# Kernel optimization log

Hardware: AMD Instinct MI355X
Metric: run time of the kernel (lower is better)

Reference implementation:

```python
import jax, jax.numpy as jnp
import numpy as np

IN_DIM, OUT_DIM, HID, L, PRED_LEN = 6, 6, 512, 4, 10


def _rnn_layer(x, Wih, Whh, bih, bhh):
    """Vanilla tanh RNN layer, batch_first x: [B,T,D] -> ([B,T,H], hT [B,H])."""
    B = x.shape[0]
    H = Whh.shape[0]
    xW = jnp.einsum('btd,hd->bth', x, Wih) + bih  # precompute input projections

    def step(h, xw_t):
        h = jnp.tanh(xw_t + h @ Whh.T + bhh)
        return h, h

    h0 = jnp.zeros((B, H), x.dtype)
    hT, ys = jax.lax.scan(step, h0, jnp.swapaxes(xW, 0, 1))
    return jnp.swapaxes(ys, 0, 1), hT


def setup_inputs() -> dict:
    key = jax.random.key(0)
    ks = jax.random.split(key, 16)
    s_in = 1.0 / np.sqrt(HID)
    u = lambda k, shp: jax.random.uniform(k, shp, jnp.float32, -s_in, s_in)
    inp = {
        'x': jax.random.normal(ks[0], (1024, 128, IN_DIM), jnp.float32),
        # encoder RNN params (layer 0 has input_dim=6, layers 1..3 have HID)
        'enc_Wih0': u(ks[1], (HID, IN_DIM)),
        'enc_Wih': u(ks[2], (L - 1, HID, HID)),
        'enc_Whh': u(ks[3], (L, HID, HID)),
        'enc_bih': u(ks[4], (L, HID)),
        'enc_bhh': u(ks[5], (L, HID)),
        # decoder RNN params (all layers take HID-dim input)
        'dec_Wih': u(ks[6], (L, HID, HID)),
        'dec_Whh': u(ks[7], (L, HID, HID)),
        'dec_bih': u(ks[8], (L, HID)),
        'dec_bhh': u(ks[9], (L, HID)),
        # output head
        'fc_W': u(ks[10], (OUT_DIM, HID)),
        'fc_b': u(ks[11], (OUT_DIM,)),
    }
    return inp


def reference(x, enc_Wih0, enc_Wih, enc_Whh, enc_bih, enc_bhh,
              dec_Wih, dec_Whh, dec_bih, dec_bhh, fc_W, fc_b):
    B = x.shape[0]
    # ---- encoder: 4-layer tanh RNN over src sequence ----
    h_enc = []
    out = x
    for l in range(L):
        Wih = enc_Wih0 if l == 0 else enc_Wih[l - 1]
        out, hT = _rnn_layer(out, Wih, enc_Whh[l], enc_bih[l], enc_bhh[l])
        h_enc.append(hT)
    enc_outputs = out                      # [B, T_src, HID]
    hidden = jnp.stack(h_enc)              # [L, B, HID]

    de_input0 = enc_outputs[:, -1, :]      # [B, HID]

    def dec_step(carry, _):
        inp, h = carry
        x_l = inp
        new_h = []
        for l in range(L):
            hl = jnp.tanh(x_l @ dec_Wih[l].T + dec_bih[l]
                          + h[l] @ dec_Whh[l].T + dec_bhh[l])
            new_h.append(hl)
            x_l = hl
        return (x_l, jnp.stack(new_h)), x_l

    _, ys = jax.lax.scan(dec_step, (de_input0, hidden), None, length=PRED_LEN)
    dec_out = jnp.swapaxes(ys, 0, 1)       # [B, PRED_LEN, HID]
    outputs = dec_out @ fc_W.T + fc_b      # [B, PRED_LEN, OUT_DIM]
    return enc_outputs, outputs
```

## Files before the change

kernel.cpp:

```cpp
#include <hip/hip_runtime.h>

typedef _Float16 f16;
typedef _Float16 f16x8 __attribute__((ext_vector_type(8)));
typedef float    f32x4 __attribute__((ext_vector_type(4)));
typedef unsigned long long u64;

#define TSEQ 128
#define PRED 10

__global__ void k_cvt(const float* __restrict__ src, f16* __restrict__ dst, int n) {
  int i = blockIdx.x * blockDim.x + threadIdx.x;
  int stride = gridDim.x * blockDim.x;
  for (; i < n; i += stride) dst[i] = (f16)src[i];
}

__global__ void k_bias(const float* __restrict__ a, const float* __restrict__ b,
                       float* __restrict__ o, int n) {
  int i = blockIdx.x * blockDim.x + threadIdx.x;
  if (i < n) o[i] = a[i] + b[i];
}

__global__ __launch_bounds__(256) void k_gemm_xw(
    const f16* __restrict__ A, const f16* __restrict__ W,
    const float* __restrict__ bias, f16* __restrict__ C) {
  __shared__ f16 As[128 * 72];
  __shared__ f16 Bs[256 * 72];
  const int tid = threadIdx.x;
  const int w = tid >> 6, lane = tid & 63;
  const int wm = w >> 1, wn = w & 1;
  const int q = lane >> 4, l15 = lane & 15;
  const int m0 = blockIdx.x * 128;
  const int n0 = blockIdx.y * 256;

  f32x4 acc[4][8];
  const f32x4 zero = {0.f, 0.f, 0.f, 0.f};
#pragma unroll
  for (int i = 0; i < 4; i++)
#pragma unroll
    for (int j = 0; j < 8; j++) acc[i][j] = zero;

  for (int k0 = 0; k0 < 512; k0 += 64) {
    __syncthreads();
#pragma unroll
    for (int i = 0; i < 4; i++) {
      int ch = tid + 256 * i; int r = ch >> 3, kc = ch & 7;
      *(f16x8*)&As[r * 72 + kc * 8] = *(const f16x8*)&A[(size_t)(m0 + r) * 512 + k0 + kc * 8];
    }
#pragma unroll
    for (int i = 0; i < 8; i++) {
      int ch = tid + 256 * i; int r = ch >> 3, kc = ch & 7;
      *(f16x8*)&Bs[r * 72 + kc * 8] = *(const f16x8*)&W[(size_t)(n0 + r) * 512 + k0 + kc * 8];
    }
    __syncthreads();
#pragma unroll
    for (int kk = 0; kk < 2; kk++) {
      f16x8 af[4], bf[8];
#pragma unroll
      for (int mt = 0; mt < 4; mt++)
        af[mt] = *(const f16x8*)&As[(wm * 64 + mt * 16 + l15) * 72 + kk * 32 + q * 8];
#pragma unroll
      for (int nt = 0; nt < 8; nt++)
        bf[nt] = *(const f16x8*)&Bs[(wn * 128 + nt * 16 + l15) * 72 + kk * 32 + q * 8];
#pragma unroll
      for (int mt = 0; mt < 4; mt++)
#pragma unroll
        for (int nt = 0; nt < 8; nt++)
          acc[mt][nt] = __builtin_amdgcn_mfma_f32_16x16x32_f16(af[mt], bf[nt], acc[mt][nt], 0, 0, 0);
    }
  }
#pragma unroll
  for (int mt = 0; mt < 4; mt++)
#pragma unroll
    for (int nt = 0; nt < 8; nt++)
#pragma unroll
      for (int r = 0; r < 4; r++) {
        int mg = m0 + wm * 64 + mt * 16 + q * 4 + r;
        int ng = n0 + wn * 128 + nt * 16 + l15;
        C[(size_t)mg * 512 + ng] = (f16)(acc[mt][nt][r] + bias[ng]);
      }
}

__global__ __launch_bounds__(256) void k_enc_rec(
    const f16* __restrict__ xw, const float* __restrict__ x,
    const float* __restrict__ Wih0, const float* __restrict__ bias0,
    const f16* __restrict__ Whh, f16* __restrict__ out_h,
    float* __restrict__ out_f, f16* __restrict__ hT,
    f16* __restrict__ hx, int* __restrict__ ctr, int is_l0) {
  __shared__ f16 As[16 * 520];
  __shared__ float xs[16][8];
  const int tid = threadIdx.x;
  const int w = tid >> 6, lane = tid & 63, q = lane >> 4, l15 = lane & 15;
  const int c = blockIdx.x & 63, sub = blockIdx.x >> 6;
  const int row0 = c * 16;
  const int ncol0 = sub * 128 + w * 32;
  int* myctr = ctr + c * 32;

  f16x8 Bfr[2][16];
#pragma unroll
  for (int t2 = 0; t2 < 2; t2++) {
    int ng = ncol0 + t2 * 16 + l15;
#pragma unroll
    for (int kk = 0; kk < 16; kk++)
      Bfr[t2][kk] = *(const f16x8*)&Whh[(size_t)ng * 512 + kk * 32 + q * 8];
  }

  float w0[2][6]; float b0[2];
  if (is_l0) {
#pragma unroll
    for (int t2 = 0; t2 < 2; t2++) {
      int ng = ncol0 + t2 * 16 + l15;
#pragma unroll
      for (int d = 0; d < 6; d++) w0[t2][d] = Wih0[ng * 6 + d];
      b0[t2] = bias0[ng];
    }
  }

  for (int i = tid; i < 16 * 520; i += 256) As[i] = (f16)0.0f;
  if (is_l0 && tid < 96) xs[tid / 6][tid % 6] = x[(size_t)(row0 + tid / 6) * TSEQ * 6 + tid % 6];
  __syncthreads();

  for (int t = 0; t < TSEQ; t++) {
    const int p = t & 1;
    f16 xwr[2][4];
    if (!is_l0) {
#pragma unroll
      for (int t2 = 0; t2 < 2; t2++)
#pragma unroll
        for (int r = 0; r < 4; r++)
          xwr[t2][r] = xw[((size_t)(row0 + q * 4 + r) * TSEQ + t) * 512 + ncol0 + t2 * 16 + l15];
    }

    const f32x4 zero = {0.f, 0.f, 0.f, 0.f};
    f32x4 acc0 = zero, acc1 = zero;
#pragma unroll
    for (int kk = 0; kk < 16; kk++) {
      f16x8 a = *(const f16x8*)&As[l15 * 520 + kk * 32 + q * 8];
      acc0 = __builtin_amdgcn_mfma_f32_16x16x32_f16(a, Bfr[0][kk], acc0, 0, 0, 0);
      acc1 = __builtin_amdgcn_mfma_f32_16x16x32_f16(a, Bfr[1][kk], acc1, 0, 0, 0);
    }

    float hv[2][4];
    union { u64 u; f16 h4[4]; } pk[2];
#pragma unroll
    for (int t2 = 0; t2 < 2; t2++) {
      f32x4 accv = t2 ? acc1 : acc0;
#pragma unroll
      for (int r = 0; r < 4; r++) {
        int m = q * 4 + r;
        float pre;
        if (is_l0) {
          float xwv = b0[t2];
#pragma unroll
          for (int d = 0; d < 6; d++) xwv += xs[m][d] * w0[t2][d];
          pre = accv[r] + xwv;
        } else {
          pre = accv[r] + (float)xwr[t2][r];
        }
        hv[t2][r] = tanhf(pre);
        pk[t2].h4[r] = (f16)hv[t2][r];
      }
    }

    if (t < TSEQ - 1) {
#pragma unroll
      for (int t2 = 0; t2 < 2; t2++) {
        int ng = ncol0 + t2 * 16 + l15;
        __hip_atomic_store(
            (u64*)&hx[(((size_t)p * 64 + c) * 512 + ng) * 16 + q * 4],
            pk[t2].u, __ATOMIC_RELAXED, __HIP_MEMORY_SCOPE_AGENT);
      }
      __builtin_amdgcn_s_waitcnt(0);
      __syncthreads();
      if (tid == 0)
        __hip_atomic_fetch_add(myctr, 1, __ATOMIC_RELAXED, __HIP_MEMORY_SCOPE_AGENT);
    }

#pragma unroll
    for (int t2 = 0; t2 < 2; t2++) {
      int ng = ncol0 + t2 * 16 + l15;
#pragma unroll
      for (int r = 0; r < 4; r++) {
        int b = row0 + q * 4 + r;
        out_h[((size_t)b * TSEQ + t) * 512 + ng] = pk[t2].h4[r];
        if (out_f) out_f[((size_t)b * TSEQ + t) * 512 + ng] = hv[t2][r];
        if (t == TSEQ - 1) hT[(size_t)b * 512 + ng] = pk[t2].h4[r];
      }
    }
    if (t == TSEQ - 1) break;

    if (tid == 0) {
      int target = 4 * (t + 1);
      while (__hip_atomic_load(myctr, __ATOMIC_RELAXED, __HIP_MEMORY_SCOPE_AGENT) < target)
        __builtin_amdgcn_s_sleep(1);
    }
    __syncthreads();

    {
      u64 v[8];
#pragma unroll
      for (int cc = 0; cc < 2; cc++) {
        int col = tid * 2 + cc;
        const u64* bp = (const u64*)&hx[(((size_t)p * 64 + c) * 512 + col) * 16];
#pragma unroll
        for (int j = 0; j < 4; j++)
          v[cc * 4 + j] = __hip_atomic_load(bp + j, __ATOMIC_RELAXED, __HIP_MEMORY_SCOPE_AGENT);
      }
      union { u64 u[4]; f16 h[16]; } un0, un1;
      un0.u[0] = v[0]; un0.u[1] = v[1]; un0.u[2] = v[2]; un0.u[3] = v[3];
      un1.u[0] = v[4]; un1.u[1] = v[5]; un1.u[2] = v[6]; un1.u[3] = v[7];
#pragma unroll
      for (int k = 0; k < 16; k++) {
        union { f16 h2[2]; unsigned int u; } pw;
        pw.h2[0] = un0.h[k]; pw.h2[1] = un1.h[k];
        *(unsigned int*)&As[k * 520 + tid * 2] = pw.u;
      }
    }
    if (is_l0 && tid < 96)
      xs[tid / 6][tid % 6] = x[((size_t)(row0 + tid / 6) * TSEQ + (t + 1)) * 6 + tid % 6];
    __syncthreads();
  }
}

__global__ __launch_bounds__(256) void k_dec_rec(
    const f16* __restrict__ Wih, const f16* __restrict__ Whh,
    const float* __restrict__ decB, const f16* __restrict__ hT,
    f16* __restrict__ hstate, f16* __restrict__ dec_out, int* __restrict__ ctr) {
  __shared__ f16 xb[16 * 520];
  __shared__ f16 hb[16 * 520];
  const int tid = threadIdx.x;
  const int w = tid >> 6, lane = tid & 63, q = lane >> 4, l15 = lane & 15;
  const int c = blockIdx.x >> 2, sub = blockIdx.x & 3;
  const int row0 = c * 16;
  const int ncol0 = sub * 128 + w * 32;
  int* myctr = ctr + c * 32;
  const size_t LSZ = (size_t)1024 * 512;

  auto load_rm = [&](f16* dst, const f16* src) {
#pragma unroll
    for (int i = 0; i < 4; i++) {
      int idx = tid + 256 * i; int m = idx >> 6, kc = idx & 63;
      *(f16x8*)&dst[m * 520 + kc * 8] = *(const f16x8*)&src[(size_t)(row0 + m) * 512 + kc * 8];
    }
  };
  auto load_cm = [&](f16* dst, int buf) {
    u64 v[8];
#pragma unroll
    for (int cc = 0; cc < 2; cc++) {
      int col = tid * 2 + cc;
      const u64* bp = (const u64*)&hstate[(((size_t)buf * 64 + c) * 512 + col) * 16];
#pragma unroll
      for (int j = 0; j < 4; j++)
        v[cc * 4 + j] = __hip_atomic_load(bp + j, __ATOMIC_RELAXED, __HIP_MEMORY_SCOPE_AGENT);
    }
    union { u64 u[4]; f16 h[16]; } un0, un1;
    un0.u[0] = v[0]; un0.u[1] = v[1]; un0.u[2] = v[2]; un0.u[3] = v[3];
    un1.u[0] = v[4]; un1.u[1] = v[5]; un1.u[2] = v[6]; un1.u[3] = v[7];
#pragma unroll
    for (int k = 0; k < 16; k++) {
      union { f16 h2[2]; unsigned int u; } pw;
      pw.h2[0] = un0.h[k]; pw.h2[1] = un1.h[k];
      *(unsigned int*)&dst[k * 520 + tid * 2] = pw.u;
    }
  };

  for (int s = 0; s < PRED; s++) {
    int wb = (s + 1) & 1, rb = s & 1;
    for (int l = 0; l < 4; l++) {
      const bool last = (s == PRED - 1) && (l == 3);
      if (l == 0) {
        if (s == 0) load_rm(xb, hT + 3 * LSZ);
        else load_cm(xb, rb * 4 + 3);
      } else {
        load_cm(xb, wb * 4 + (l - 1));
      }
      if (s == 0) load_rm(hb, hT + (size_t)l * LSZ);
      else load_cm(hb, rb * 4 + l);
      __syncthreads();

      const f32x4 zero = {0.f, 0.f, 0.f, 0.f};
      f32x4 acc0 = zero, acc1 = zero;
      const f16* Wl = Wih + (size_t)l * 512 * 512;
      const f16* Ul = Whh + (size_t)l * 512 * 512;
      int ng0 = ncol0 + l15, ng1 = ncol0 + 16 + l15;
#pragma unroll
      for (int kk = 0; kk < 16; kk++) {
        f16x8 a = *(const f16x8*)&xb[l15 * 520 + kk * 32 + q * 8];
        f16x8 bv0 = *(const f16x8*)&Wl[(size_t)ng0 * 512 + kk * 32 + q * 8];
        f16x8 bv1 = *(const f16x8*)&Wl[(size_t)ng1 * 512 + kk * 32 + q * 8];
        acc0 = __builtin_amdgcn_mfma_f32_16x16x32_f16(a, bv0, acc0, 0, 0, 0);
        acc1 = __builtin_amdgcn_mfma_f32_16x16x32_f16(a, bv1, acc1, 0, 0, 0);
      }
#pragma unroll
      for (int kk = 0; kk < 16; kk++) {
        f16x8 a = *(const f16x8*)&hb[l15 * 520 + kk * 32 + q * 8];
        f16x8 bv0 = *(const f16x8*)&Ul[(size_t)ng0 * 512 + kk * 32 + q * 8];
        f16x8 bv1 = *(const f16x8*)&Ul[(size_t)ng1 * 512 + kk * 32 + q * 8];
        acc0 = __builtin_amdgcn_mfma_f32_16x16x32_f16(a, bv0, acc0, 0, 0, 0);
        acc1 = __builtin_amdgcn_mfma_f32_16x16x32_f16(a, bv1, acc1, 0, 0, 0);
      }

      int obuf = wb * 4 + l;
      union { u64 u; f16 h4[4]; } pk[2];
#pragma unroll
      for (int t2 = 0; t2 < 2; t2++) {
        f32x4 accv = t2 ? acc1 : acc0;
        int ng = ncol0 + t2 * 16 + l15;
#pragma unroll
        for (int r = 0; r < 4; r++)
          pk[t2].h4[r] = (f16)tanhf(accv[r] + decB[l * 512 + ng]);
      }

      if (!last) {
#pragma unroll
        for (int t2 = 0; t2 < 2; t2++) {
          int ng = ncol0 + t2 * 16 + l15;
          __hip_atomic_store(
              (u64*)&hstate[(((size_t)obuf * 64 + c) * 512 + ng) * 16 + q * 4],
              pk[t2].u, __ATOMIC_RELAXED, __HIP_MEMORY_SCOPE_AGENT);
        }
        __builtin_amdgcn_s_waitcnt(0);
        __syncthreads();
        if (tid == 0)
          __hip_atomic_fetch_add(myctr, 1, __ATOMIC_RELAXED, __HIP_MEMORY_SCOPE_AGENT);
      }

      if (l == 3) {
#pragma unroll
        for (int t2 = 0; t2 < 2; t2++) {
          int ng = ncol0 + t2 * 16 + l15;
#pragma unroll
          for (int r = 0; r < 4; r++)
            dec_out[((size_t)(row0 + q * 4 + r) * PRED + s) * 512 + ng] = pk[t2].h4[r];
        }
      }

      if (!last) {
        if (tid == 0) {
          int target = 4 * (s * 4 + l + 1);
          while (__hip_atomic_load(myctr, __ATOMIC_RELAXED, __HIP_MEMORY_SCOPE_AGENT) < target)
            __builtin_amdgcn_s_sleep(1);
        }
        __syncthreads();
      }
    }
  }
}

__global__ __launch_bounds__(256) void k_fc(
    const f16* __restrict__ dec_out, const float* __restrict__ fcW,
    const float* __restrict__ fcb, float* __restrict__ out) {
  __shared__ float Wl[6 * 512];
  __shared__ float bl[8];
  int tid = threadIdx.x;
  for (int i = tid; i < 3072; i += 256) Wl[i] = fcW[i];
  if (tid < 6) bl[tid] = fcb[tid];
  __syncthreads();
  int g = blockIdx.x * 256 + tid;
  const f16* row = dec_out + (size_t)g * 512;
  float acc[6] = {0, 0, 0, 0, 0, 0};
  for (int kc = 0; kc < 64; kc++) {
    f16x8 xv = *(const f16x8*)&row[kc * 8];
#pragma unroll
    for (int j = 0; j < 8; j++) {
      float xf = (float)xv[j];
#pragma unroll
      for (int o = 0; o < 6; o++) acc[o] += xf * Wl[o * 512 + kc * 8 + j];
    }
  }
#pragma unroll
  for (int o = 0; o < 6; o++) out[(size_t)g * 6 + o] = acc[o] + bl[o];
}

extern "C" void kernel_launch(void* const* d_in, const int* in_sizes, int n_in,
                              void* d_out, int out_size, void* d_ws, size_t ws_size,
                              hipStream_t stream) {
  const float* x      = (const float*)d_in[0];
  const float* Wih0   = (const float*)d_in[1];
  const float* eWih32 = (const float*)d_in[2];
  const float* eWhh32 = (const float*)d_in[3];
  const float* ebih   = (const float*)d_in[4];
  const float* ebhh   = (const float*)d_in[5];
  const float* dWih32 = (const float*)d_in[6];
  const float* dWhh32 = (const float*)d_in[7];
  const float* dbih   = (const float*)d_in[8];
  const float* dbhh   = (const float*)d_in[9];
  const float* fcW    = (const float*)d_in[10];
  const float* fcb    = (const float*)d_in[11];
  float* outp = (float*)d_out;

  char* ws = (char*)d_ws;
  size_t off = 0;
  auto alloc = [&](size_t bytes) { void* p = ws + off; off += (bytes + 255) & ~255ULL; return p; };
  f16* outA   = (f16*)alloc((size_t)131072 * 512 * 2);
  f16* xwB    = (f16*)alloc((size_t)131072 * 512 * 2);
  f16* eWih   = (f16*)alloc((size_t)3 * 262144 * 2);
  f16* eWhh   = (f16*)alloc((size_t)4 * 262144 * 2);
  f16* dWih   = (f16*)alloc((size_t)4 * 262144 * 2);
  f16* dWhh   = (f16*)alloc((size_t)4 * 262144 * 2);
  float* encB = (float*)alloc(2048 * 4);
  float* decB = (float*)alloc(2048 * 4);
  f16* hT     = (f16*)alloc((size_t)4 * 1024 * 512 * 2);
  f16* hstate = (f16*)alloc((size_t)8 * 1024 * 512 * 2);
  f16* hx     = (f16*)alloc((size_t)2 * 1024 * 512 * 2);
  f16* dec_o  = (f16*)alloc((size_t)1024 * 10 * 512 * 2);
  int* ctr    = (int*)alloc(5 * 64 * 32 * 4);

  hipMemsetAsync(ctr, 0, 5 * 64 * 32 * 4, stream);
  k_cvt<<<512, 256, 0, stream>>>(eWih32, eWih, 3 * 262144);
  k_cvt<<<512, 256, 0, stream>>>(eWhh32, eWhh, 4 * 262144);
  k_cvt<<<512, 256, 0, stream>>>(dWih32, dWih, 4 * 262144);
  k_cvt<<<512, 256, 0, stream>>>(dWhh32, dWhh, 4 * 262144);
  k_bias<<<8, 256, 0, stream>>>(ebih, ebhh, encB, 2048);
  k_bias<<<8, 256, 0, stream>>>(dbih, dbhh, decB, 2048);

  k_enc_rec<<<256, 256, 0, stream>>>(nullptr, x, Wih0, encB, eWhh, outA, nullptr, hT, hx, ctr, 1);
  for (int l = 1; l < 4; l++) {
    k_gemm_xw<<<dim3(1024, 2), 256, 0, stream>>>(outA, eWih + (size_t)(l - 1) * 262144,
                                                 encB + l * 512, xwB);
    float* of = (l == 3) ? outp : nullptr;
    k_enc_rec<<<256, 256, 0, stream>>>(xwB, nullptr, nullptr, nullptr,
                                       eWhh + (size_t)l * 262144, outA, of,
                                       hT + (size_t)l * 524288, hx, ctr + l * 2048, 0);
  }
  k_dec_rec<<<256, 256, 0, stream>>>(dWih, dWhh, decB, hT, hstate, dec_o, ctr + 4 * 2048);
  k_fc<<<40, 256, 0, stream>>>(dec_o, fcW, fcb, outp + (size_t)1024 * 128 * 512);
}
```

Before: 3.151 ms.

## Replace counter barriers with tagged-data flag polling in recurrent kernels

```diff
diff --git a/kernel.cpp b/kernel.cpp
--- a/kernel.cpp
+++ b/kernel.cpp
@@ -7,6 +7,15 @@
 
 #define TSEQ 128
 #define PRED 10
+
+#define TAG_MASK (~((1ull << 62) | (1ull << 46)))
+
+static __device__ __forceinline__ u64 tag_or_bits(unsigned tg) {
+  return ((u64)(tg >> 1) << 62) | ((u64)(tg & 1) << 46);
+}
+static __device__ __forceinline__ int tag_ok(u64 w, unsigned tg) {
+  return ((unsigned)((w >> 62) & 1) == (tg >> 1)) & ((unsigned)((w >> 46) & 1) == (tg & 1));
+}
 
 __global__ void k_cvt(const float* __restrict__ src, f16* __restrict__ dst, int n) {
   int i = blockIdx.x * blockDim.x + threadIdx.x;
@@ -85,7 +94,7 @@
     const float* __restrict__ Wih0, const float* __restrict__ bias0,
     const f16* __restrict__ Whh, f16* __restrict__ out_h,
     float* __restrict__ out_f, f16* __restrict__ hT,
-    f16* __restrict__ hx, int* __restrict__ ctr, int is_l0) {
+    f16* __restrict__ hx, int is_l0) {
   __shared__ f16 As[16 * 520];
   __shared__ float xs[16][8];
   const int tid = threadIdx.x;
@@ -93,7 +102,6 @@
   const int c = blockIdx.x & 63, sub = blockIdx.x >> 6;
   const int row0 = c * 16;
   const int ncol0 = sub * 128 + w * 32;
-  int* myctr = ctr + c * 32;
 
   f16x8 Bfr[2][16];
 #pragma unroll
@@ -121,6 +129,7 @@
 
   for (int t = 0; t < TSEQ; t++) {
     const int p = t & 1;
+    const unsigned tg = (unsigned)((t >> 1) & 3);
     f16 xwr[2][4];
     if (!is_l0) {
 #pragma unroll
@@ -162,17 +171,14 @@
     }
 
     if (t < TSEQ - 1) {
+      const u64 tor = tag_or_bits(tg);
 #pragma unroll
       for (int t2 = 0; t2 < 2; t2++) {
         int ng = ncol0 + t2 * 16 + l15;
         __hip_atomic_store(
             (u64*)&hx[(((size_t)p * 64 + c) * 512 + ng) * 16 + q * 4],
-            pk[t2].u, __ATOMIC_RELAXED, __HIP_MEMORY_SCOPE_AGENT);
-      }
-      __builtin_amdgcn_s_waitcnt(0);
-      __syncthreads();
-      if (tid == 0)
-        __hip_atomic_fetch_add(myctr, 1, __ATOMIC_RELAXED, __HIP_MEMORY_SCOPE_AGENT);
+            pk[t2].u | tor, __ATOMIC_RELAXED, __HIP_MEMORY_SCOPE_AGENT);
+      }
     }
 
 #pragma unroll
@@ -188,26 +194,24 @@
     }
     if (t == TSEQ - 1) break;
 
-    if (tid == 0) {
-      int target = 4 * (t + 1);
-      while (__hip_atomic_load(myctr, __ATOMIC_RELAXED, __HIP_MEMORY_SCOPE_AGENT) < target)
-        __builtin_amdgcn_s_sleep(1);
+    u64 v[8];
+    {
+      const u64* base = (const u64*)hx + ((size_t)p * 64 + c) * 2048 + (size_t)tid * 8;
+      unsigned pend = 0xFFu;
+      do {
+#pragma unroll
+        for (int i = 0; i < 8; i++) if (pend & (1u << i)) {
+          u64 wv = __hip_atomic_load(base + i, __ATOMIC_RELAXED, __HIP_MEMORY_SCOPE_AGENT);
+          if (tag_ok(wv, tg)) { v[i] = wv; pend &= ~(1u << i); }
+        }
+        if (pend) __builtin_amdgcn_s_sleep(1);
+      } while (pend);
     }
     __syncthreads();
-
     {
-      u64 v[8];
-#pragma unroll
-      for (int cc = 0; cc < 2; cc++) {
-        int col = tid * 2 + cc;
-        const u64* bp = (const u64*)&hx[(((size_t)p * 64 + c) * 512 + col) * 16];
-#pragma unroll
-        for (int j = 0; j < 4; j++)
-          v[cc * 4 + j] = __hip_atomic_load(bp + j, __ATOMIC_RELAXED, __HIP_MEMORY_SCOPE_AGENT);
-      }
       union { u64 u[4]; f16 h[16]; } un0, un1;
-      un0.u[0] = v[0]; un0.u[1] = v[1]; un0.u[2] = v[2]; un0.u[3] = v[3];
-      un1.u[0] = v[4]; un1.u[1] = v[5]; un1.u[2] = v[6]; un1.u[3] = v[7];
+#pragma unroll
+      for (int j = 0; j < 4; j++) { un0.u[j] = v[j] & TAG_MASK; un1.u[j] = v[4 + j] & TAG_MASK; }
 #pragma unroll
       for (int k = 0; k < 16; k++) {
         union { f16 h2[2]; unsigned int u; } pw;
@@ -224,7 +228,7 @@
 __global__ __launch_bounds__(256) void k_dec_rec(
     const f16* __restrict__ Wih, const f16* __restrict__ Whh,
     const float* __restrict__ decB, const f16* __restrict__ hT,
-    f16* __restrict__ hstate, f16* __restrict__ dec_out, int* __restrict__ ctr) {
+    f16* __restrict__ hstate, f16* __restrict__ dec_out) {
   __shared__ f16 xb[16 * 520];
   __shared__ f16 hb[16 * 520];
   const int tid = threadIdx.x;
@@ -232,7 +236,6 @@
   const int c = blockIdx.x >> 2, sub = blockIdx.x & 3;
   const int row0 = c * 16;
   const int ncol0 = sub * 128 + w * 32;
-  int* myctr = ctr + c * 32;
   const size_t LSZ = (size_t)1024 * 512;
 
   auto load_rm = [&](f16* dst, const f16* src) {
@@ -242,19 +245,10 @@
       *(f16x8*)&dst[m * 520 + kc * 8] = *(const f16x8*)&src[(size_t)(row0 + m) * 512 + kc * 8];
     }
   };
-  auto load_cm = [&](f16* dst, int buf) {
-    u64 v[8];
-#pragma unroll
-    for (int cc = 0; cc < 2; cc++) {
-      int col = tid * 2 + cc;
-      const u64* bp = (const u64*)&hstate[(((size_t)buf * 64 + c) * 512 + col) * 16];
-#pragma unroll
-      for (int j = 0; j < 4; j++)
-        v[cc * 4 + j] = __hip_atomic_load(bp + j, __ATOMIC_RELAXED, __HIP_MEMORY_SCOPE_AGENT);
-    }
+  auto unpack_lds = [&](f16* dst, const u64* v) {
     union { u64 u[4]; f16 h[16]; } un0, un1;
-    un0.u[0] = v[0]; un0.u[1] = v[1]; un0.u[2] = v[2]; un0.u[3] = v[3];
-    un1.u[0] = v[4]; un1.u[1] = v[5]; un1.u[2] = v[6]; un1.u[3] = v[7];
+#pragma unroll
+    for (int j = 0; j < 4; j++) { un0.u[j] = v[j] & TAG_MASK; un1.u[j] = v[4 + j] & TAG_MASK; }
 #pragma unroll
     for (int k = 0; k < 16; k++) {
       union { f16 h2[2]; unsigned int u; } pw;
@@ -262,19 +256,53 @@
       *(unsigned int*)&dst[k * 520 + tid * 2] = pw.u;
     }
   };
+  auto load_cm = [&](f16* dst, int buf, unsigned tg) {
+    u64 v[8];
+    const u64* base = (const u64*)hstate + ((size_t)buf * 64 + c) * 2048 + (size_t)tid * 8;
+    unsigned pend = 0xFFu;
+    do {
+#pragma unroll
+      for (int i = 0; i < 8; i++) if (pend & (1u << i)) {
+        u64 wv = __hip_atomic_load(base + i, __ATOMIC_RELAXED, __HIP_MEMORY_SCOPE_AGENT);
+        if (tag_ok(wv, tg)) { v[i] = wv; pend &= ~(1u << i); }
+      }
+      if (pend) __builtin_amdgcn_s_sleep(1);
+    } while (pend);
+    unpack_lds(dst, v);
+  };
+  auto load_cm2 = [&](int bufx, unsigned tgx, int bufh, unsigned tgh) {
+    u64 v[16];
+    const u64* bx = (const u64*)hstate + ((size_t)bufx * 64 + c) * 2048 + (size_t)tid * 8;
+    const u64* bh = (const u64*)hstate + ((size_t)bufh * 64 + c) * 2048 + (size_t)tid * 8;
+    unsigned pend = 0xFFFFu;
+    do {
+#pragma unroll
+      for (int i = 0; i < 16; i++) if (pend & (1u << i)) {
+        const u64* bp = (i < 8) ? bx : bh;
+        unsigned tg = (i < 8) ? tgx : tgh;
+        u64 wv = __hip_atomic_load(bp + (i & 7), __ATOMIC_RELAXED, __HIP_MEMORY_SCOPE_AGENT);
+        if (tag_ok(wv, tg)) { v[i] = wv; pend &= ~(1u << i); }
+      }
+      if (pend) __builtin_amdgcn_s_sleep(1);
+    } while (pend);
+    unpack_lds(xb, v);
+    unpack_lds(hb, v + 8);
+  };
 
   for (int s = 0; s < PRED; s++) {
     int wb = (s + 1) & 1, rb = s & 1;
     for (int l = 0; l < 4; l++) {
       const bool last = (s == PRED - 1) && (l == 3);
-      if (l == 0) {
-        if (s == 0) load_rm(xb, hT + 3 * LSZ);
-        else load_cm(xb, rb * 4 + 3);
+      if (s == 0) {
+        if (l == 0) load_rm(xb, hT + 3 * LSZ);
+        else        load_cm(xb, wb * 4 + (l - 1), 0u);
+        load_rm(hb, hT + (size_t)l * LSZ);
       } else {
-        load_cm(xb, wb * 4 + (l - 1));
-      }
-      if (s == 0) load_rm(hb, hT + (size_t)l * LSZ);
-      else load_cm(hb, rb * 4 + l);
+        unsigned tgp = (unsigned)(((s - 1) >> 1) & 3);
+        unsigned tgc = (unsigned)((s >> 1) & 3);
+        if (l == 0) load_cm2(rb * 4 + 3, tgp, rb * 4 + 0, tgp);
+        else        load_cm2(wb * 4 + (l - 1), tgc, rb * 4 + l, tgp);
+      }
       __syncthreads();
 
       const f32x4 zero = {0.f, 0.f, 0.f, 0.f};
@@ -311,17 +339,14 @@
       }
 
       if (!last) {
+        const u64 tor = tag_or_bits((unsigned)((s >> 1) & 3));
 #pragma unroll
         for (int t2 = 0; t2 < 2; t2++) {
           int ng = ncol0 + t2 * 16 + l15;
           __hip_atomic_store(
               (u64*)&hstate[(((size_t)obuf * 64 + c) * 512 + ng) * 16 + q * 4],
-              pk[t2].u, __ATOMIC_RELAXED, __HIP_MEMORY_SCOPE_AGENT);
+              pk[t2].u | tor, __ATOMIC_RELAXED, __HIP_MEMORY_SCOPE_AGENT);
         }
-        __builtin_amdgcn_s_waitcnt(0);
-        __syncthreads();
-        if (tid == 0)
-          __hip_atomic_fetch_add(myctr, 1, __ATOMIC_RELAXED, __HIP_MEMORY_SCOPE_AGENT);
       }
 
       if (l == 3) {
@@ -334,14 +359,7 @@
         }
       }
 
-      if (!last) {
-        if (tid == 0) {
-          int target = 4 * (s * 4 + l + 1);
-          while (__hip_atomic_load(myctr, __ATOMIC_RELAXED, __HIP_MEMORY_SCOPE_AGENT) < target)
-            __builtin_amdgcn_s_sleep(1);
-        }
-        __syncthreads();
-      }
+      if (!last) __syncthreads();
     }
   }
 }
@@ -403,9 +421,10 @@
   f16* hstate = (f16*)alloc((size_t)8 * 1024 * 512 * 2);
   f16* hx     = (f16*)alloc((size_t)2 * 1024 * 512 * 2);
   f16* dec_o  = (f16*)alloc((size_t)1024 * 10 * 512 * 2);
-  int* ctr    = (int*)alloc(5 * 64 * 32 * 4);
-
-  hipMemsetAsync(ctr, 0, 5 * 64 * 32 * 4, stream);
+
+  hipMemsetAsync(hx, 0xFF, (size_t)2 * 1024 * 512 * 2, stream);
+  hipMemsetAsync(hstate, 0xFF, (size_t)8 * 1024 * 512 * 2, stream);
+
   k_cvt<<<512, 256, 0, stream>>>(eWih32, eWih, 3 * 262144);
   k_cvt<<<512, 256, 0, stream>>>(eWhh32, eWhh, 4 * 262144);
   k_cvt<<<512, 256, 0, stream>>>(dWih32, dWih, 4 * 262144);
@@ -413,15 +432,15 @@
   k_bias<<<8, 256, 0, stream>>>(ebih, ebhh, encB, 2048);
   k_bias<<<8, 256, 0, stream>>>(dbih, dbhh, decB, 2048);
 
-  k_enc_rec<<<256, 256, 0, stream>>>(nullptr, x, Wih0, encB, eWhh, outA, nullptr, hT, hx, ctr, 1);
+  k_enc_rec<<<256, 256, 0, stream>>>(nullptr, x, Wih0, encB, eWhh, outA, nullptr, hT, hx, 1);
   for (int l = 1; l < 4; l++) {
     k_gemm_xw<<<dim3(1024, 2), 256, 0, stream>>>(outA, eWih + (size_t)(l - 1) * 262144,
                                                  encB + l * 512, xwB);
     float* of = (l == 3) ? outp : nullptr;
     k_enc_rec<<<256, 256, 0, stream>>>(xwB, nullptr, nullptr, nullptr,
                                        eWhh + (size_t)l * 262144, outA, of,
-                                       hT + (size_t)l * 524288, hx, ctr + l * 2048, 0);
-  }
-  k_dec_rec<<<256, 256, 0, stream>>>(dWih, dWhh, decB, hT, hstate, dec_o, ctr + 4 * 2048);
+                                       hT + (size_t)l * 524288, hx, 0);
+  }
+  k_dec_rec<<<256, 256, 0, stream>>>(dWih, dWhh, decB, hT, hstate, dec_o);
   k_fc<<<40, 256, 0, stream>>>(dec_o, fcW, fcb, outp + (size_t)1024 * 128 * 512);
 }
```

Result: no change. 3.208 ms (+1.8%).

## Fuse all encoder layers into one wavefront-pipelined persistent kernel with xW ring buffers

Applied to the files above, without the earlier changes.

```diff
diff --git a/kernel.cpp b/kernel.cpp
--- a/kernel.cpp
+++ b/kernel.cpp
@@ -20,80 +20,33 @@
   if (i < n) o[i] = a[i] + b[i];
 }
 
-__global__ __launch_bounds__(256) void k_gemm_xw(
-    const f16* __restrict__ A, const f16* __restrict__ W,
-    const float* __restrict__ bias, f16* __restrict__ C) {
-  __shared__ f16 As[128 * 72];
-  __shared__ f16 Bs[256 * 72];
-  const int tid = threadIdx.x;
-  const int w = tid >> 6, lane = tid & 63;
-  const int wm = w >> 1, wn = w & 1;
-  const int q = lane >> 4, l15 = lane & 15;
-  const int m0 = blockIdx.x * 128;
-  const int n0 = blockIdx.y * 256;
-
-  f32x4 acc[4][8];
-  const f32x4 zero = {0.f, 0.f, 0.f, 0.f};
-#pragma unroll
-  for (int i = 0; i < 4; i++)
-#pragma unroll
-    for (int j = 0; j < 8; j++) acc[i][j] = zero;
-
-  for (int k0 = 0; k0 < 512; k0 += 64) {
-    __syncthreads();
-#pragma unroll
-    for (int i = 0; i < 4; i++) {
-      int ch = tid + 256 * i; int r = ch >> 3, kc = ch & 7;
-      *(f16x8*)&As[r * 72 + kc * 8] = *(const f16x8*)&A[(size_t)(m0 + r) * 512 + k0 + kc * 8];
-    }
-#pragma unroll
-    for (int i = 0; i < 8; i++) {
-      int ch = tid + 256 * i; int r = ch >> 3, kc = ch & 7;
-      *(f16x8*)&Bs[r * 72 + kc * 8] = *(const f16x8*)&W[(size_t)(n0 + r) * 512 + k0 + kc * 8];
-    }
-    __syncthreads();
-#pragma unroll
-    for (int kk = 0; kk < 2; kk++) {
-      f16x8 af[4], bf[8];
-#pragma unroll
-      for (int mt = 0; mt < 4; mt++)
-        af[mt] = *(const f16x8*)&As[(wm * 64 + mt * 16 + l15) * 72 + kk * 32 + q * 8];
-#pragma unroll
-      for (int nt = 0; nt < 8; nt++)
-        bf[nt] = *(const f16x8*)&Bs[(wn * 128 + nt * 16 + l15) * 72 + kk * 32 + q * 8];
-#pragma unroll
-      for (int mt = 0; mt < 4; mt++)
-#pragma unroll
-        for (int nt = 0; nt < 8; nt++)
-          acc[mt][nt] = __builtin_amdgcn_mfma_f32_16x16x32_f16(af[mt], bf[nt], acc[mt][nt], 0, 0, 0);
-    }
-  }
-#pragma unroll
-  for (int mt = 0; mt < 4; mt++)
-#pragma unroll
-    for (int nt = 0; nt < 8; nt++)
-#pragma unroll
-      for (int r = 0; r < 4; r++) {
-        int mg = m0 + wm * 64 + mt * 16 + q * 4 + r;
-        int ng = n0 + wn * 128 + nt * 16 + l15;
-        C[(size_t)mg * 512 + ng] = (f16)(acc[mt][nt][r] + bias[ng]);
-      }
-}
-
-__global__ __launch_bounds__(256) void k_enc_rec(
-    const f16* __restrict__ xw, const float* __restrict__ x,
-    const float* __restrict__ Wih0, const float* __restrict__ bias0,
-    const f16* __restrict__ Whh, f16* __restrict__ out_h,
-    float* __restrict__ out_f, f16* __restrict__ hT,
-    f16* __restrict__ hx, int* __restrict__ ctr, int is_l0) {
+__global__ __launch_bounds__(256, 4) void k_enc_wave(
+    const float* __restrict__ x, const float* __restrict__ Wih0,
+    const f16* __restrict__ eWih, const float* __restrict__ encB,
+    const f16* __restrict__ eWhh, float* __restrict__ out_f,
+    f16* __restrict__ hT, f16* __restrict__ hx, f16* __restrict__ xwring,
+    int* __restrict__ ctr, int* __restrict__ pf, int* __restrict__ cp) {
   __shared__ f16 As[16 * 520];
   __shared__ float xs[16][8];
   const int tid = threadIdx.x;
   const int w = tid >> 6, lane = tid & 63, q = lane >> 4, l15 = lane & 15;
-  const int c = blockIdx.x & 63, sub = blockIdx.x >> 6;
-  const int row0 = c * 16;
-  const int ncol0 = sub * 128 + w * 32;
-  int* myctr = ctr + c * 32;
+  const int bid = blockIdx.x;
+  const int layer = bid & 3, sub = (bid >> 2) & 3, c = bid >> 4;
+  const int row0 = c * 16, ncol0 = sub * 128 + w * 32;
+  const int is_l0 = (layer == 0), is_top = (layer == 3);
+  int* myctr = ctr + (layer * 64 + c) * 32;
+  const f16* Whh = eWhh + (size_t)layer * 262144;
+  f16* myhx = hx + (size_t)layer * (2 * 64 * 8192);
+  f16* myhT = hT + (size_t)layer * ((size_t)1024 * 512);
+
+  const int ci = is_l0 ? 0 : (layer - 1);
+  u64* crng = (u64*)(xwring + (size_t)ci * 64 * 16 * 8192);
+  int* cpf = pf + ((ci * 64 + c) * 4 + sub) * 8;
+  int* ccp = cp + ((ci * 64 + c) * 4 + sub) * 8;
+  u64* prng = (u64*)(xwring + (size_t)layer * 64 * 16 * 8192);
+  int* ppf = pf + ((layer * 64 + c) * 4 + sub) * 8;
+  int* pcp = cp + ((layer * 64 + c) * 4 + sub) * 8;
+  const f16* Wt = eWih + (size_t)layer * 262144;
 
   f16x8 Bfr[2][16];
 #pragma unroll
@@ -111,8 +64,13 @@
       int ng = ncol0 + t2 * 16 + l15;
 #pragma unroll
       for (int d = 0; d < 6; d++) w0[t2][d] = Wih0[ng * 6 + d];
-      b0[t2] = bias0[ng];
-    }
+      b0[t2] = encB[ng];
+    }
+  }
+  float tb[2] = {0.f, 0.f};
+  if (!is_top) {
+    tb[0] = encB[(layer + 1) * 512 + ncol0 + l15];
+    tb[1] = encB[(layer + 1) * 512 + ncol0 + 16 + l15];
   }
 
   for (int i = tid; i < 16 * 520; i += 256) As[i] = (f16)0.0f;
@@ -121,14 +79,6 @@
 
   for (int t = 0; t < TSEQ; t++) {
     const int p = t & 1;
-    f16 xwr[2][4];
-    if (!is_l0) {
-#pragma unroll
-      for (int t2 = 0; t2 < 2; t2++)
-#pragma unroll
-        for (int r = 0; r < 4; r++)
-          xwr[t2][r] = xw[((size_t)(row0 + q * 4 + r) * TSEQ + t) * 512 + ncol0 + t2 * 16 + l15];
-    }
 
     const f32x4 zero = {0.f, 0.f, 0.f, 0.f};
     f32x4 acc0 = zero, acc1 = zero;
@@ -137,6 +87,18 @@
       f16x8 a = *(const f16x8*)&As[l15 * 520 + kk * 32 + q * 8];
       acc0 = __builtin_amdgcn_mfma_f32_16x16x32_f16(a, Bfr[0][kk], acc0, 0, 0, 0);
       acc1 = __builtin_amdgcn_mfma_f32_16x16x32_f16(a, Bfr[1][kk], acc1, 0, 0, 0);
+    }
+
+    f16 xwr[2][4];
+    if (!is_l0) {
+      while (__hip_atomic_load(cpf, __ATOMIC_RELAXED, __HIP_MEMORY_SCOPE_AGENT) < t + 1)
+        __builtin_amdgcn_s_sleep(1);
+      u64* rb = crng + ((size_t)c * 16 + (t & 15)) * 2048;
+      union { u64 u; f16 h[4]; } a0, a1;
+      a0.u = __hip_atomic_load(rb + (size_t)(ncol0 + l15) * 4 + q, __ATOMIC_RELAXED, __HIP_MEMORY_SCOPE_AGENT);
+      a1.u = __hip_atomic_load(rb + (size_t)(ncol0 + 16 + l15) * 4 + q, __ATOMIC_RELAXED, __HIP_MEMORY_SCOPE_AGENT);
+#pragma unroll
+      for (int r = 0; r < 4; r++) { xwr[0][r] = a0.h[r]; xwr[1][r] = a1.h[r]; }
     }
 
     float hv[2][4];
@@ -161,31 +123,71 @@
       }
     }
 
-    if (t < TSEQ - 1) {
+    const bool pub = (t < TSEQ - 1) || !is_top;
+    if (pub) {
 #pragma unroll
       for (int t2 = 0; t2 < 2; t2++) {
         int ng = ncol0 + t2 * 16 + l15;
         __hip_atomic_store(
-            (u64*)&hx[(((size_t)p * 64 + c) * 512 + ng) * 16 + q * 4],
+            (u64*)&myhx[(((size_t)p * 64 + c) * 512 + ng) * 16 + q * 4],
             pk[t2].u, __ATOMIC_RELAXED, __HIP_MEMORY_SCOPE_AGENT);
       }
+      __builtin_amdgcn_s_waitcnt(0);
+      __syncthreads();
+      if (tid == 0) {
+        __hip_atomic_fetch_add(myctr, 1, __ATOMIC_RELAXED, __HIP_MEMORY_SCOPE_AGENT);
+        if (!is_l0)
+          __hip_atomic_store(ccp, t + 1, __ATOMIC_RELAXED, __HIP_MEMORY_SCOPE_AGENT);
+      }
+    }
+
+    if (is_top) {
+#pragma unroll
+      for (int t2 = 0; t2 < 2; t2++) {
+        int ng = ncol0 + t2 * 16 + l15;
+#pragma unroll
+        for (int r = 0; r < 4; r++)
+          out_f[((size_t)(row0 + q * 4 + r) * TSEQ + t) * 512 + ng] = hv[t2][r];
+      }
+    }
+    if (t == TSEQ - 1) {
+#pragma unroll
+      for (int t2 = 0; t2 < 2; t2++) {
+        int ng = ncol0 + t2 * 16 + l15;
+#pragma unroll
+        for (int r = 0; r < 4; r++)
+          myhT[(size_t)(row0 + q * 4 + r) * 512 + ng] = pk[t2].h4[r];
+      }
+    }
+
+    if (!is_top && t >= 1) {
+      if (t >= 17)
+        while (__hip_atomic_load(pcp, __ATOMIC_RELAXED, __HIP_MEMORY_SCOPE_AGENT) < t - 16)
+          __builtin_amdgcn_s_sleep(1);
+      f32x4 xa0 = zero, xa1 = zero;
+#pragma unroll
+      for (int kk = 0; kk < 16; kk++) {
+        f16x8 a = *(const f16x8*)&As[l15 * 520 + kk * 32 + q * 8];
+        f16x8 bv0 = *(const f16x8*)&Wt[(size_t)(ncol0 + l15) * 512 + kk * 32 + q * 8];
+        f16x8 bv1 = *(const f16x8*)&Wt[(size_t)(ncol0 + 16 + l15) * 512 + kk * 32 + q * 8];
+        xa0 = __builtin_amdgcn_mfma_f32_16x16x32_f16(a, bv0, xa0, 0, 0, 0);
+        xa1 = __builtin_amdgcn_mfma_f32_16x16x32_f16(a, bv1, xa1, 0, 0, 0);
+      }
+      union { u64 u; f16 h4[4]; } qk[2];
+#pragma unroll
+      for (int r = 0; r < 4; r++) {
+        qk[0].h4[r] = (f16)(xa0[r] + tb[0]);
+        qk[1].h4[r] = (f16)(xa1[r] + tb[1]);
+      }
+      u64* rb = prng + ((size_t)c * 16 + ((t - 1) & 15)) * 2048;
+      __hip_atomic_store(rb + (size_t)(ncol0 + l15) * 4 + q, qk[0].u, __ATOMIC_RELAXED, __HIP_MEMORY_SCOPE_AGENT);
+      __hip_atomic_store(rb + (size_t)(ncol0 + 16 + l15) * 4 + q, qk[1].u, __ATOMIC_RELAXED, __HIP_MEMORY_SCOPE_AGENT);
       __builtin_amdgcn_s_waitcnt(0);
       __syncthreads();
       if (tid == 0)
-        __hip_atomic_fetch_add(myctr, 1, __ATOMIC_RELAXED, __HIP_MEMORY_SCOPE_AGENT);
-    }
-
-#pragma unroll
-    for (int t2 = 0; t2 < 2; t2++) {
-      int ng = ncol0 + t2 * 16 + l15;
-#pragma unroll
-      for (int r = 0; r < 4; r++) {
-        int b = row0 + q * 4 + r;
-        out_h[((size_t)b * TSEQ + t) * 512 + ng] = pk[t2].h4[r];
-        if (out_f) out_f[((size_t)b * TSEQ + t) * 512 + ng] = hv[t2][r];
-        if (t == TSEQ - 1) hT[(size_t)b * 512 + ng] = pk[t2].h4[r];
-      }
-    }
+        __hip_atomic_store(ppf, t, __ATOMIC_RELAXED, __HIP_MEMORY_SCOPE_AGENT);
+    }
+
     if (t == TSEQ - 1) break;
 
     if (tid == 0) {
@@ -194,13 +196,12 @@
         __builtin_amdgcn_s_sleep(1);
     }
     __syncthreads();
-
     {
       u64 v[8];
 #pragma unroll
       for (int cc = 0; cc < 2; cc++) {
         int col = tid * 2 + cc;
-        const u64* bp = (const u64*)&hx[(((size_t)p * 64 + c) * 512 + col) * 16];
+        const u64* bp = (const u64*)&myhx[(((size_t)p * 64 + c) * 512 + col) * 16];
 #pragma unroll
         for (int j = 0; j < 4; j++)
           v[cc * 4 + j] = __hip_atomic_load(bp + j, __ATOMIC_RELAXED, __HIP_MEMORY_SCOPE_AGENT);
@@ -218,6 +219,60 @@
     if (is_l0 && tid < 96)
       xs[tid / 6][tid % 6] = x[((size_t)(row0 + tid / 6) * TSEQ + (t + 1)) * 6 + tid % 6];
     __syncthreads();
+  }
+
+  if (!is_top) {
+    if (tid == 0) {
+      while (__hip_atomic_load(myctr, __ATOMIC_RELAXED, __HIP_MEMORY_SCOPE_AGENT) < 4 * TSEQ)
+        __builtin_amdgcn_s_sleep(1);
+    }
+    __syncthreads();
+    {
+      u64 v[8];
+#pragma unroll
+      for (int cc = 0; cc < 2; cc++) {
+        int col = tid * 2 + cc;
+        const u64* bp = (const u64*)&myhx[(((size_t)1 * 64 + c) * 512 + col) * 16];
+#pragma unroll
+        for (int j = 0; j < 4; j++)
+          v[cc * 4 + j] = __hip_atomic_load(bp + j, __ATOMIC_RELAXED, __HIP_MEMORY_SCOPE_AGENT);
+      }
+      union { u64 u[4]; f16 h[16]; } un0, un1;
+      un0.u[0] = v[0]; un0.u[1] = v[1]; un0.u[2] = v[2]; un0.u[3] = v[3];
+      un1.u[0] = v[4]; un1.u[1] = v[5]; un1.u[2] = v[6]; un1.u[3] = v[7];
+#pragma unroll
+      for (int k = 0; k < 16; k++) {
+        union { f16 h2[2]; unsigned int u; } pw;
+        pw.h2[0] = un0.h[k]; pw.h2[1] = un1.h[k];
+        *(unsigned int*)&As[k * 520 + tid * 2] = pw.u;
+      }
+    }
+    __syncthreads();
+    while (__hip_atomic_load(pcp, __ATOMIC_RELAXED, __HIP_MEMORY_SCOPE_AGENT) < TSEQ - 16)
+      __builtin_amdgcn_s_sleep(1);
+    const f32x4 zero = {0.f, 0.f, 0.f, 0.f};
+    f32x4 xa0 = zero, xa1 = zero;
+#pragma unroll
+    for (int kk = 0; kk < 16; kk++) {
+      f16x8 a = *(const f16x8*)&As[l15 * 520 + kk * 32 + q * 8];
+      f16x8 bv0 = *(const f16x8*)&Wt[(size_t)(ncol0 + l15) * 512 + kk * 32 + q * 8];
+      f16x8 bv1 = *(const f16x8*)&Wt[(size_t)(ncol0 + 16 + l15) * 512 + kk * 32 + q * 8];
+      xa0 = __builtin_amdgcn_mfma_f32_16x16x32_f16(a, bv0, xa0, 0, 0, 0);
+      xa1 = __builtin_amdgcn_mfma_f32_16x16x32_f16(a, bv1, xa1, 0, 0, 0);
+    }
+    union { u64 u; f16 h4[4]; } qk[2];
+#pragma unroll
+    for (int r = 0; r < 4; r++) {
+      qk[0].h4[r] = (f16)(xa0[r] + tb[0]);
+      qk[1].h4[r] = (f16)(xa1[r] + tb[1]);
+    }
+    u64* rb = prng + ((size_t)c * 16 + 15) * 2048;
+    __hip_atomic_store(rb + (size_t)(ncol0 + l15) * 4 + q, qk[0].u, __ATOMIC_RELAXED, __HIP_MEMORY_SCOPE_AGENT);
+    __hip_atomic_store(rb + (size_t)(ncol0 + 16 + l15) * 4 + q, qk[1].u, __ATOMIC_RELAXED, __HIP_MEMORY_SCOPE_AGENT);
+    __builtin_amdgcn_s_waitcnt(0);
+    __syncthreads();
+    if (tid == 0)
+      __hip_atomic_store(ppf, TSEQ, __ATOMIC_RELAXED, __HIP_MEMORY_SCOPE_AGENT);
   }
 }
 
@@ -391,8 +446,6 @@
   char* ws = (char*)d_ws;
   size_t off = 0;
   auto alloc = [&](size_t bytes) { void* p = ws + off; off += (bytes + 255) & ~255ULL; return p; };
-  f16* outA   = (f16*)alloc((size_t)131072 * 512 * 2);
-  f16* xwB    = (f16*)alloc((size_t)131072 * 512 * 2);
   f16* eWih   = (f16*)alloc((size_t)3 * 262144 * 2);
   f16* eWhh   = (f16*)alloc((size_t)4 * 262144 * 2);
   f16* dWih   = (f16*)alloc((size_t)4 * 262144 * 2);
@@ -401,11 +454,17 @@
   float* decB = (float*)alloc(2048 * 4);
   f16* hT     = (f16*)alloc((size_t)4 * 1024 * 512 * 2);
   f16* hstate = (f16*)alloc((size_t)8 * 1024 * 512 * 2);
-  f16* hx     = (f16*)alloc((size_t)2 * 1024 * 512 * 2);
+  f16* hx     = (f16*)alloc((size_t)4 * 2 * 64 * 8192 * 2);
+  f16* xwring = (f16*)alloc((size_t)3 * 64 * 16 * 8192 * 2);
   f16* dec_o  = (f16*)alloc((size_t)1024 * 10 * 512 * 2);
-  int* ctr    = (int*)alloc(5 * 64 * 32 * 4);
-
-  hipMemsetAsync(ctr, 0, 5 * 64 * 32 * 4, stream);
+  int* ctrE   = (int*)alloc(4 * 64 * 32 * 4);
+  int* ctrD   = (int*)alloc(64 * 32 * 4);
+  int* pfA    = (int*)alloc(3 * 64 * 4 * 8 * 4);
+  int* cpA    = (int*)alloc(3 * 64 * 4 * 8 * 4);
+
+  size_t syncsz = (char*)(cpA + 3 * 64 * 4 * 8) - (char*)ctrE;
+  hipMemsetAsync(ctrE, 0, syncsz, stream);
+
   k_cvt<<<512, 256, 0, stream>>>(eWih32, eWih, 3 * 262144);
   k_cvt<<<512, 256, 0, stream>>>(eWhh32, eWhh, 4 * 262144);
   k_cvt<<<512, 256, 0, stream>>>(dWih32, dWih, 4 * 262144);
@@ -413,15 +472,8 @@
   k_bias<<<8, 256, 0, stream>>>(ebih, ebhh, encB, 2048);
   k_bias<<<8, 256, 0, stream>>>(dbih, dbhh, decB, 2048);
 
-  k_enc_rec<<<256, 256, 0, stream>>>(nullptr, x, Wih0, encB, eWhh, outA, nullptr, hT, hx, ctr, 1);
-  for (int l = 1; l < 4; l++) {
-    k_gemm_xw<<<dim3(1024, 2), 256, 0, stream>>>(outA, eWih + (size_t)(l - 1) * 262144,
-                                                 encB + l * 512, xwB);
-    float* of = (l == 3) ? outp : nullptr;
-    k_enc_rec<<<256, 256, 0, stream>>>(xwB, nullptr, nullptr, nullptr,
-                                       eWhh + (size_t)l * 262144, outA, of,
-                                       hT + (size_t)l * 524288, hx, ctr + l * 2048, 0);
-  }
-  k_dec_rec<<<256, 256, 0, stream>>>(dWih, dWhh, decB, hT, hstate, dec_o, ctr + 4 * 2048);
+  k_enc_wave<<<1024, 256, 0, stream>>>(x, Wih0, eWih, encB, eWhh, outp, hT, hx,
+                                       xwring, ctrE, pfA, cpA);
+  k_dec_rec<<<256, 256, 0, stream>>>(dWih, dWhh, decB, hT, hstate, dec_o, ctrD);
   k_fc<<<40, 256, 0, stream>>>(dec_o, fcW, fcb, outp + (size_t)1024 * 128 * 512);
 }
```

Measured after the change: 4.875 ms. 54.7% more time.
